# Kernel tuning notes

Hardware: AMD Instinct MI355X
Metric: run time of the kernel (lower is better)

## Reference

```python
import jax, jax.numpy as jnp
import numpy as np
import math

B, S, E = 2, 2048, 1024
H, D = 16, 64
LAMBDA_INIT = 0.8
GN_EPS = 1e-5


def setup_inputs() -> dict:
    key = jax.random.key(0)
    ks = jax.random.split(key, 12)
    s = 0.02
    inputs = jax.random.normal(ks[0], (B, S, E), jnp.float32)
    attention_mask = jnp.ones((B, S), jnp.float32)
    token_indices = jnp.sort(jax.random.randint(ks[1], (B, S), 0, S), axis=-1)
    Wq = jax.random.normal(ks[2], (2 * H * D, E), jnp.float32) * s
    Wk = jax.random.normal(ks[3], (2 * H * D, E), jnp.float32) * s
    Wv = jax.random.normal(ks[4], (H * D, E), jnp.float32) * s
    Wo = jax.random.normal(ks[5], (E, H * D), jnp.float32) * s
    lam_q1 = jax.random.normal(ks[6], (D,), jnp.float32) * 0.1
    lam_q2 = jax.random.normal(ks[7], (D,), jnp.float32) * 0.1
    lam_k1 = jax.random.normal(ks[8], (D,), jnp.float32) * 0.1
    lam_k2 = jax.random.normal(ks[9], (D,), jnp.float32) * 0.1
    gn_w = jnp.ones((H * D,), jnp.float32)
    gn_b = jnp.zeros((H * D,), jnp.float32)
    return dict(inputs=inputs, attention_mask=attention_mask, token_indices=token_indices,
                Wq=Wq, Wk=Wk, Wv=Wv, Wo=Wo,
                lam_q1=lam_q1, lam_q2=lam_q2, lam_k1=lam_k1, lam_k2=lam_k2,
                gn_w=gn_w, gn_b=gn_b)


def reference(inputs, attention_mask, token_indices, Wq, Wk, Wv, Wo,
              lam_q1, lam_q2, lam_k1, lam_k2, gn_w, gn_b):
    b, s, e = inputs.shape
    # projections: q,k have doubled head dim (differential), v is standard
    q = (inputs @ Wq.T).reshape(b, s, H, 2 * D).transpose(0, 2, 1, 3)  # [B,H,S,2D]
    k = (inputs @ Wk.T).reshape(b, s, H, 2 * D).transpose(0, 2, 1, 3)
    v = (inputs @ Wv.T).reshape(b, s, H, D).transpose(0, 2, 1, 3)      # [B,H,S,D]
    Q1, Q2 = q[..., :D], q[..., D:]
    K1, K2 = k[..., :D], k[..., D:]
    scale = 1.0 / math.sqrt(D)
    s1 = jnp.einsum('bhqd,bhkd->bhqk', Q1, K1) * scale
    s2 = jnp.einsum('bhqd,bhkd->bhqk', Q2, K2) * scale
    # ALiBi bias: slopes[h] * (pos_q - pos_k), subtracted
    slopes = 2.0 ** (-8.0 * jnp.arange(1, H + 1, dtype=jnp.float32) / H)
    pos = token_indices.astype(jnp.float32)                            # [B,S]
    pos_diff = pos[:, :, None] - pos[:, None, :]                       # [B,S,S]
    bias = slopes[None, :, None, None] * pos_diff[:, None, :, :]       # [B,H,S,S]
    # causal + padding masks
    causal = jnp.triu(jnp.full((s, s), -1e9, jnp.float32), 1)[None, None]
    pad = (1.0 - attention_mask)[:, None, None, :] * -1e9
    s1 = s1 - bias + causal + pad
    s2 = s2 - bias + causal + pad
    w1 = jax.nn.softmax(s1, axis=-1)
    w2 = jax.nn.softmax(s2, axis=-1)
    lam = jnp.exp(jnp.dot(lam_q1, lam_k1)) - jnp.exp(jnp.dot(lam_q2, lam_k2)) + LAMBDA_INIT
    w = w1 - lam * w2
    out = jnp.einsum('bhqk,bhkd->bhqd', w, v)                          # [B,H,S,D]
    # GroupNorm(num_groups=H, num_channels=H*D) over channels-first layout [B,C,S]
    x = out.transpose(0, 2, 1, 3).reshape(b, s, H * D).transpose(0, 2, 1)  # [B,C,S]
    xg = x.reshape(b, H, D * s)
    mean = xg.mean(axis=-1, keepdims=True)
    var = xg.var(axis=-1, keepdims=True)
    xn = ((xg - mean) / jnp.sqrt(var + GN_EPS)).reshape(b, H * D, s)
    xn = xn * gn_w[None, :, None] + gn_b[None, :, None]
    xn = xn * (1.0 - LAMBDA_INIT)
    attn = xn.transpose(0, 2, 1)                                       # [B,S,H*D]
    return attn @ Wo.T
```

## Files before the change

### kernel.cpp

```cpp
#include <hip/hip_runtime.h>
#include <hip/hip_bf16.h>

typedef __hip_bfloat16 bf16;
typedef float f32x4 __attribute__((ext_vector_type(4)));
typedef float fvec4 __attribute__((ext_vector_type(4)));
typedef short s16x8 __attribute__((ext_vector_type(8)));

#define NB_B 2
#define NB_S 2048
#define NB_E 1024
#define NB_H 16
#define NB_D 64

typedef const __attribute__((address_space(1))) void* GPTR;
typedef __attribute__((address_space(3))) void* LPTR;

__device__ __forceinline__ void gld16(const void* g, void* l) {
  __builtin_amdgcn_global_load_lds((GPTR)g, (LPTR)l, 16, 0, 0);
}

__device__ __forceinline__ s16x8 ld8(const bf16* p) { return *(const s16x8*)p; }

__device__ __forceinline__ f32x4 MFMA(s16x8 a, s16x8 b, f32x4 c) {
  return __builtin_amdgcn_mfma_f32_16x16x32_bf16(a, b, c, 0, 0, 0);
}

struct __align__(8) bf16x4 { bf16 a, b, c, d; };

__global__ void prep_kernel(const float* __restrict__ inputs,
                            const float* __restrict__ wq, const float* __restrict__ wk,
                            const float* __restrict__ wv, const float* __restrict__ wo,
                            const float* __restrict__ lq1, const float* __restrict__ lq2,
                            const float* __restrict__ lk1, const float* __restrict__ lk2,
                            bf16* __restrict__ xbf,
                            bf16* __restrict__ oq, bf16* __restrict__ ok,
                            bf16* __restrict__ ov, bf16* __restrict__ oo,
                            float* __restrict__ lamo) {
  const int blk = blockIdx.x;
  if (blk < 4096) {
    int i = blk * 256 + threadIdx.x;
    fvec4 v = ((const fvec4*)inputs)[i];
    bf16x4 o = { bf16(v.x), bf16(v.y), bf16(v.z), bf16(v.w) };
    ((bf16x4*)xbf)[i] = o;
  } else if (blk < 10240) {
    int i = (blk - 4096) * 256 + threadIdx.x;
    const float* src; bf16* dst; int off;
    if (i < 524288)       { src = wq; dst = oq; off = i; }
    else if (i < 1048576) { src = wk; dst = ok; off = i - 524288; }
    else if (i < 1310720) { src = wv; dst = ov; off = i - 1048576; }
    else                  { src = wo; dst = oo; off = i - 1310720; }
    fvec4 v = ((const fvec4*)src)[off];
    bf16x4 o = { bf16(v.x), bf16(v.y), bf16(v.z), bf16(v.w) };
    ((bf16x4*)dst)[off] = o;
  } else {
    int l = threadIdx.x;
    if (l < 64) {
      float d1 = lq1[l] * lk1[l];
      float d2 = lq2[l] * lk2[l];
#pragma unroll
      for (int o = 32; o; o >>= 1) { d1 += __shfl_xor(d1, o); d2 += __shfl_xor(d2, o); }
      if (l == 0) lamo[0] = expf(d1) - expf(d2) + 0.8f;
    }
  }
}

__global__ void combo_kernel(const int* __restrict__ tok, const float* __restrict__ amask,
                             float* __restrict__ combo) {
  int i = blockIdx.x * 256 + threadIdx.x;
  int hh = i >> 12, bs = i & 4095;
  float slopeL = exp2f(-0.5f * (float)(hh + 1)) * 1.44269504088896340736f;
  combo[i] = slopeL * (float)tok[bs] + (amask[bs] - 1.f) * 1.44269504e9f;
}

template <int EPI>
__global__ __launch_bounds__(256) void gemm_bt(const bf16* __restrict__ A,
                                               const bf16* __restrict__ Bw,
                                               bf16* __restrict__ Ob,
                                               bf16* __restrict__ Ob2,
                                               bf16* __restrict__ Ob3,
                                               float* __restrict__ Of,
                                               int Kd, float oscale) {
  __shared__ bf16 As[2][128 * 32];
  __shared__ bf16 Bs[2][128 * 32];
  const int tid = threadIdx.x;
  const int lane = tid & 63;
  const int fr = lane & 15, fq = lane >> 4;
  const int wave = tid >> 6;
  const int wr = (wave >> 1) * 64, wc = (wave & 1) * 64;
  const size_t m0 = (size_t)blockIdx.x * 128, n0 = (size_t)blockIdx.y * 128;

  f32x4 acc[4][4];
#pragma unroll
  for (int i = 0; i < 4; i++)
#pragma unroll
    for (int j = 0; j < 4; j++) acc[i][j] = f32x4{0.f, 0.f, 0.f, 0.f};

  const int ca = tid, cb = tid + 256;
  const bf16* ga0 = A + (m0 + (ca >> 2)) * Kd + (ca & 3) * 8;
  const bf16* ga1 = A + (m0 + (cb >> 2)) * Kd + (cb & 3) * 8;
  const bf16* gb0 = Bw + (n0 + (ca >> 2)) * Kd + (ca & 3) * 8;
  const bf16* gb1 = Bw + (n0 + (cb >> 2)) * Kd + (cb & 3) * 8;

  gld16(ga0, &As[0][ca * 8]);
  gld16(ga1, &As[0][cb * 8]);
  gld16(gb0, &Bs[0][ca * 8]);
  gld16(gb1, &Bs[0][cb * 8]);
  __syncthreads();

  const int NKT = Kd >> 5;
  for (int kti = 0; kti < NKT; ++kti) {
    const int cur = kti & 1;
    if (kti + 1 < NKT) {
      const int kt = (kti + 1) << 5;
      gld16(ga0 + kt, &As[cur ^ 1][ca * 8]);
      gld16(ga1 + kt, &As[cur ^ 1][cb * 8]);
      gld16(gb0 + kt, &Bs[cur ^ 1][ca * 8]);
      gld16(gb1 + kt, &Bs[cur ^ 1][cb * 8]);
    }
    s16x8 af[4], bfv[4];
#pragma unroll
    for (int mi = 0; mi < 4; mi++) af[mi] = ld8(&As[cur][(wr + mi * 16 + fr) * 32 + fq * 8]);
#pragma unroll
    for (int ni = 0; ni < 4; ni++) bfv[ni] = ld8(&Bs[cur][(wc + ni * 16 + fr) * 32 + fq * 8]);
#pragma unroll
    for (int mi = 0; mi < 4; mi++)
#pragma unroll
      for (int ni = 0; ni < 4; ni++)
        acc[mi][ni] = MFMA(af[mi], bfv[ni], acc[mi][ni]);
    __syncthreads();
  }

  bf16* dst = Ob;
  size_t nsub = 0;
  float osc = oscale;
  bool isV = false;
  if constexpr (EPI == 0) {
    if (n0 >= 4096)      { dst = Ob3; nsub = 4096; osc = 1.0f; isV = true; }
    else if (n0 >= 2048) { dst = Ob2; nsub = 2048; osc = 1.0f; }
  }

#pragma unroll
  for (int mi = 0; mi < 4; mi++)
#pragma unroll
    for (int ni = 0; ni < 4; ni++)
#pragma unroll
      for (int i = 0; i < 4; i++) {
        size_t m = m0 + wr + mi * 16 + fq * 4 + i;
        size_t n = n0 + wc + ni * 16 + fr;
        if constexpr (EPI == 0) {
          float v = acc[mi][ni][i] * osc;
          size_t nn = n - nsub;
          size_t b = m >> 11, s = m & 2047;
          if (!isV) {
            size_t h = nn >> 7, dd = nn & 127;
            dst[((b * NB_H + h) * NB_S + s) * 128 + dd] = bf16(v);
          } else {
            size_t h = nn >> 6, d = nn & 63;
            dst[((b * NB_H + h) * NB_D + d) * NB_S + s] = bf16(v);
          }
        } else {
          Of[m * 1024 + n] = acc[mi][ni][i] * oscale;
        }
      }
}

__global__ __launch_bounds__(512, 2) void attn_kernel(
    const bf16* __restrict__ Q, const bf16* __restrict__ Kk, const bf16* __restrict__ Vt,
    const int* __restrict__ tok, const float* __restrict__ combo,
    const float* __restrict__ lamp, bf16* __restrict__ Xb, float* __restrict__ gnp) {
  __shared__ bf16 Ks[2][2][4096];
  __shared__ bf16 Vs[2][4096];
  __shared__ bf16 Ps[8][1024];
  __shared__ float gs[8][2];

  const int tid = threadIdx.x, lane = tid & 63, wave = tid >> 6;
  const int fr = lane & 15, fq = lane >> 4;
  const int id = blockIdx.x;
  const int w = id >> 3;
  const int bh = (id & 7) * 4 + (w & 3);
  const int qj = 15 - (w >> 2);
  const int b = bh >> 4, h = bh & 15;

  const float lam = lamp[0];
  const float slopeL = exp2f(-0.5f * (float)(h + 1)) * 1.44269504088896340736f;
  const float* comboH = combo + ((size_t)h * NB_B + b) * NB_S;

  const bf16* Kbase = Kk + (size_t)bh * NB_S * 128;
  const bf16* Vbase = Vt + (size_t)bh * NB_D * NB_S;

  const s16x8 onesv = { 0x3F80, 0x3F80, 0x3F80, 0x3F80, 0x3F80, 0x3F80, 0x3F80, 0x3F80 };

  const bf16* gK[2]; int lK[2];
#pragma unroll
  for (int i = 0; i < 2; i++) {
    int c = tid + i * 512, set = c >> 9, cc = c & 511;
    int row = cc >> 3, col8 = cc & 7, sc = col8 ^ (row & 7);
    gK[i] = Kbase + (size_t)row * 128 + set * 64 + sc * 8;
    lK[i] = set * 4096 + cc * 8;
  }
  const bf16* gV; int lV;
  {
    int c = tid;
    int row = c >> 3, col8 = c & 7, sc = col8 ^ (row & 7);
    gV = Vbase + (size_t)row * NB_S + sc * 8;
    lV = c * 8;
  }

  const int q0 = qj * 128;
  const int qw = q0 + wave * 16;
  const int ntiles = 2 * qj + 2;

  const bf16* qrow = Q + ((size_t)bh * NB_S + qw + fr) * 128;
  s16x8 q1[2], q2[2];
  q1[0] = ld8(qrow + fq * 8);       q1[1] = ld8(qrow + 32 + fq * 8);
  q2[0] = ld8(qrow + 64 + fq * 8);  q2[1] = ld8(qrow + 96 + fq * 8);

  const int qg = qw + fr;
  const float pq = slopeL * (float)tok[b * NB_S + qg];

  float m1 = -1e30f, m2 = -1e30f;
  f32x4 acc1[4], acc2[4];
  f32x4 accL1 = f32x4{0.f,0.f,0.f,0.f}, accL2 = f32x4{0.f,0.f,0.f,0.f};
#pragma unroll
  for (int nt = 0; nt < 4; nt++) { acc1[nt] = f32x4{0.f,0.f,0.f,0.f}; acc2[nt] = f32x4{0.f,0.f,0.f,0.f}; }

#pragma unroll
  for (int i = 0; i < 2; i++) gld16(gK[i], &Ks[0][0][0] + lK[i]);
  gld16(gV, &Vs[0][0] + lV);
  __syncthreads();

  for (int t = 0; t < ntiles; ++t) {
    const int cur = t & 1;
    const int kv0 = t * 64;
    if (t + 1 < ntiles) {
#pragma unroll
      for (int i = 0; i < 2; i++)
        gld16(gK[i] + (size_t)(kv0 + 64) * 128, &Ks[cur ^ 1][0][0] + lK[i]);
      gld16(gV + (size_t)(kv0 + 64), &Vs[cur ^ 1][0] + lV);
    }

    const bool active = (kv0 <= qw + 15);
    if (active) {
      fvec4 cmbv[4];
#pragma unroll
      for (int nt = 0; nt < 4; nt++)
        cmbv[nt] = *(const fvec4*)(comboH + kv0 + nt * 16 + fq * 4);

      f32x4 c1[4], c2[4];
#pragma unroll
      for (int nt = 0; nt < 4; nt++) { c1[nt] = f32x4{0.f,0.f,0.f,0.f}; c2[nt] = f32x4{0.f,0.f,0.f,0.f}; }
      __builtin_amdgcn_s_setprio(1);
#pragma unroll
      for (int nt = 0; nt < 4; nt++) {
        const int krow = nt * 16 + fr;
#pragma unroll
        for (int kk = 0; kk < 2; kk++) {
          const int sch = ((kk * 4 + fq) ^ (krow & 7)) * 8;
          c1[nt] = MFMA(ld8(&Ks[cur][0][krow * 64 + sch]), q1[kk], c1[nt]);
          c2[nt] = MFMA(ld8(&Ks[cur][1][krow * 64 + sch]), q2[kk], c2[nt]);
        }
      }
      __builtin_amdgcn_s_setprio(0);

      float sv1[4][4], sv2[4][4];
#pragma unroll
      for (int nt = 0; nt < 4; nt++)
#pragma unroll
        for (int i = 0; i < 4; i++) {
          const float biasv = cmbv[nt][i] - pq;
          sv1[nt][i] = c1[nt][i] + biasv;
          sv2[nt][i] = c2[nt][i] + biasv;
        }
      if (kv0 + 63 > qw) {
#pragma unroll
        for (int nt = 0; nt < 4; nt++)
#pragma unroll
          for (int i = 0; i < 4; i++)
            if (kv0 + nt * 16 + fq * 4 + i > qg) { sv1[nt][i] = -1e30f; sv2[nt][i] = -1e30f; }
      }

      s16x8 vf[4][2];
#pragma unroll
      for (int nt = 0; nt < 4; nt++) {
        const int vrow = nt * 16 + fr;
#pragma unroll
        for (int kk = 0; kk < 2; kk++)
          vf[nt][kk] = ld8(&Vs[cur][vrow * 64 + (((kk * 4 + fq) ^ (vrow & 7)) << 3)]);
      }

      {
        float pm = fmaxf(fmaxf(fmaxf(sv1[0][0], sv1[0][1]), fmaxf(sv1[0][2], sv1[0][3])),
                         fmaxf(fmaxf(sv1[1][0], sv1[1][1]), fmaxf(sv1[1][2], sv1[1][3])));
        pm = fmaxf(pm, fmaxf(fmaxf(fmaxf(sv1[2][0], sv1[2][1]), fmaxf(sv1[2][2], sv1[2][3])),
                             fmaxf(fmaxf(sv1[3][0], sv1[3][1]), fmaxf(sv1[3][2], sv1[3][3]))));
        pm = fmaxf(pm, __shfl_xor(pm, 16));
        pm = fmaxf(pm, __shfl_xor(pm, 32));
        if (__any(pm > m1 + 8.f)) {
          const float nm = fmaxf(m1, pm);
          const float cor = exp2f(m1 - nm);
          m1 = nm;
#pragma unroll
          for (int i = 0; i < 4; i++) {
            const float ci = __shfl(cor, fq * 4 + i);
            accL1[i] *= ci;
#pragma unroll
            for (int nt = 0; nt < 4; nt++) acc1[nt][i] *= ci;
          }
        }
#pragma unroll
        for (int nt = 0; nt < 4; nt++) {
          bf16x4 pk = { bf16(exp2f(sv1[nt][0] - m1)), bf16(exp2f(sv1[nt][1] - m1)),
                        bf16(exp2f(sv1[nt][2] - m1)), bf16(exp2f(sv1[nt][3] - m1)) };
          *(bf16x4*)&Ps[wave][fr * 64 + ((((nt * 4 + fq) ^ ((fr & 7) << 1))) << 2)] = pk;
        }
        __builtin_amdgcn_s_setprio(1);
#pragma unroll
        for (int kk = 0; kk < 2; kk++) {
          const s16x8 pa = ld8(&Ps[wave][fr * 64 + (((kk * 8 + fq * 2) ^ ((fr & 7) << 1)) << 2)]);
          accL1 = MFMA(pa, onesv, accL1);
#pragma unroll
          for (int nt = 0; nt < 4; nt++) acc1[nt] = MFMA(pa, vf[nt][kk], acc1[nt]);
        }
        __builtin_amdgcn_s_setprio(0);
      }
      {
        float pm = fmaxf(fmaxf(fmaxf(sv2[0][0], sv2[0][1]), fmaxf(sv2[0][2], sv2[0][3])),
                         fmaxf(fmaxf(sv2[1][0], sv2[1][1]), fmaxf(sv2[1][2], sv2[1][3])));
        pm = fmaxf(pm, fmaxf(fmaxf(fmaxf(sv2[2][0], sv2[2][1]), fmaxf(sv2[2][2], sv2[2][3])),
                             fmaxf(fmaxf(sv2[3][0], sv2[3][1]), fmaxf(sv2[3][2], sv2[3][3]))));
        pm = fmaxf(pm, __shfl_xor(pm, 16));
        pm = fmaxf(pm, __shfl_xor(pm, 32));
        if (__any(pm > m2 + 8.f)) {
          const float nm = fmaxf(m2, pm);
          const float cor = exp2f(m2 - nm);
          m2 = nm;
#pragma unroll
          for (int i = 0; i < 4; i++) {
            const float ci = __shfl(cor, fq * 4 + i);
            accL2[i] *= ci;
#pragma unroll
            for (int nt = 0; nt < 4; nt++) acc2[nt][i] *= ci;
          }
        }
#pragma unroll
        for (int nt = 0; nt < 4; nt++) {
          bf16x4 pk = { bf16(exp2f(sv2[nt][0] - m2)), bf16(exp2f(sv2[nt][1] - m2)),
                        bf16(exp2f(sv2[nt][2] - m2)), bf16(exp2f(sv2[nt][3] - m2)) };
          *(bf16x4*)&Ps[wave][fr * 64 + ((((nt * 4 + fq) ^ ((fr & 7) << 1))) << 2)] = pk;
        }
        __builtin_amdgcn_s_setprio(1);
#pragma unroll
        for (int kk = 0; kk < 2; kk++) {
          const s16x8 pa = ld8(&Ps[wave][fr * 64 + (((kk * 8 + fq * 2) ^ ((fr & 7) << 1)) << 2)]);
          accL2 = MFMA(pa, onesv, accL2);
#pragma unroll
          for (int nt = 0; nt < 4; nt++) acc2[nt] = MFMA(pa, vf[nt][kk], acc2[nt]);
        }
        __builtin_amdgcn_s_setprio(0);
      }
    }

    __syncthreads();
  }

  float r1b[4], r2b[4];
#pragma unroll
  for (int i = 0; i < 4; i++) { r1b[i] = 1.f / accL1[i]; r2b[i] = lam / accL2[i]; }
  float s = 0.f, s2 = 0.f;
#pragma unroll
  for (int nt = 0; nt < 4; nt++)
#pragma unroll
    for (int i = 0; i < 4; i++) {
      const float v = acc1[nt][i] * r1b[i] - acc2[nt][i] * r2b[i];
      Xb[((size_t)bh * NB_S + qw + fq * 4 + i) * NB_D + nt * 16 + fr] = bf16(v);
      s += v; s2 += v * v;
    }
#pragma unroll
  for (int o = 32; o; o >>= 1) { s += __shfl_xor(s, o); s2 += __shfl_xor(s2, o); }
  if (lane == 0) { gs[wave][0] = s; gs[wave][1] = s2; }
  __syncthreads();
  if (tid == 0) {
    float S = 0.f, S2 = 0.f;
#pragma unroll
    for (int i = 0; i < 8; i++) { S += gs[i][0]; S2 += gs[i][1]; }
    atomicAdd(&gnp[bh * 2], S);
    atomicAdd(&gnp[bh * 2 + 1], S2);
  }
}

__global__ __launch_bounds__(256) void gn_apply(const bf16* __restrict__ Xb,
                                                const float* __restrict__ gnp,
                                                const float* __restrict__ gw,
                                                const float* __restrict__ gb,
                                                bf16* __restrict__ Xn) {
  const int blk = blockIdx.x, bh = blk >> 3, seg = blk & 7;
  const int b = bh >> 4, h = bh & 15;
  const float mean = gnp[bh * 2] * (1.f / 131072.f);
  const float var = gnp[bh * 2 + 1] * (1.f / 131072.f) - mean * mean;
  const float rstd = rsqrtf(var + 1e-5f) * 0.2f;
  const int tid = threadIdx.x;
  const int d0 = (tid * 8) & 63;
  const int c = h * 64 + d0;
  fvec4 w0 = *(const fvec4*)(gw + c), w1 = *(const fvec4*)(gw + c + 4);
  fvec4 b0 = *(const fvec4*)(gb + c), b1 = *(const fvec4*)(gb + c + 4);
  float wv[8] = { w0.x, w0.y, w0.z, w0.w, w1.x, w1.y, w1.z, w1.w };
  float bv[8] = { b0.x, b0.y, b0.z, b0.w, b1.x, b1.y, b1.z, b1.w };
  const bf16* xp = Xb + (size_t)bh * 131072;
#pragma unroll
  for (int j = 0; j < 8; j++) {
    const int e = seg * 16384 + (tid + j * 256) * 8;
    const int srow = e >> 6;
    s16x8 xv = *(const s16x8*)(xp + e);
    bf16 o8[8];
#pragma unroll
    for (int k = 0; k < 8; k++) {
      const float xf = __uint_as_float(((unsigned)(unsigned short)xv[k]) << 16);
      o8[k] = bf16((xf - mean) * rstd * wv[k] + 0.2f * bv[k]);
    }
    *(s16x8*)(Xn + ((size_t)b * NB_S + srow) * 1024 + c) = *(const s16x8*)o8;
  }
}

extern "C" void kernel_launch(void* const* d_in, const int* in_sizes, int n_in,
                              void* d_out, int out_size, void* d_ws, size_t ws_size,
                              hipStream_t stream) {
  const float* inputs = (const float*)d_in[0];
  const float* amask  = (const float*)d_in[1];
  const int*   tok    = (const int*)d_in[2];
  const float* Wq = (const float*)d_in[3];
  const float* Wk = (const float*)d_in[4];
  const float* Wv = (const float*)d_in[5];
  const float* Wo = (const float*)d_in[6];
  const float* lq1 = (const float*)d_in[7];
  const float* lq2 = (const float*)d_in[8];
  const float* lk1 = (const float*)d_in[9];
  const float* lk2 = (const float*)d_in[10];
  const float* gw = (const float*)d_in[11];
  const float* gb = (const float*)d_in[12];
  float* out = (float*)d_out;
  char* ws = (char*)d_ws;

  bf16* Xbf = (bf16*)(ws + 0);
  bf16* Wqb = (bf16*)(ws + 8388608);
  bf16* Wkb = (bf16*)(ws + 12582912);
  bf16* Wvb = (bf16*)(ws + 16777216);
  bf16* Xb  = (bf16*)(ws + 0);
  float* combo = (float*)(ws + 16777216);
  bf16* Qb  = (bf16*)(ws + 18874368);
  bf16* Xn  = (bf16*)(ws + 18874368);
  bf16* Kb  = (bf16*)(ws + 35651584);
  bf16* Vtb = (bf16*)(ws + 52428800);
  bf16* Wob = (bf16*)(ws + 60817408);
  float* lam = (float*)(ws + 62914560);
  float* gnp = (float*)(ws + 62914816);

  const float QSCALE = 0.125f * 1.44269504088896340736f;

  (void)hipMemsetAsync(gnp, 0, 512, stream);
  prep_kernel<<<10241, 256, 0, stream>>>(inputs, Wq, Wk, Wv, Wo, lq1, lq2, lk1, lk2,
                                         Xbf, Wqb, Wkb, Wvb, Wob, lam);

  gemm_bt<0><<<dim3(32, 40), 256, 0, stream>>>(Xbf, Wqb, Qb, Kb, Vtb, nullptr, 1024, QSCALE);

  combo_kernel<<<256, 256, 0, stream>>>(tok, amask, combo);

  attn_kernel<<<512, 512, 0, stream>>>(Qb, Kb, Vtb, tok, combo, lam, Xb, gnp);

  gn_apply<<<256, 256, 0, stream>>>(Xb, gnp, gw, gb, Xn);

  gemm_bt<2><<<dim3(32, 8), 256, 0, stream>>>(Xn, Wob, nullptr, nullptr, nullptr, out, 1024, 1.0f);
}
```

Measured before the change: 217.1 us.

## Fold ALiBi bias into MFMA accumulator init and remap GEMM blocks per XCD

In the attention kernel, the per-query ALiBi term is dropped, since a constant shift per row leaves the softmax unchanged. The score accumulators are seeded with the per-key combo bias, and the combo values for the next tile are prefetched into registers alongside the K/V loads. This removes the separate bias-add pass and the tok load. The GEMM kernels move to a 1D grid whose block index is remapped so each XCD works on a contiguous slice of N columns, aiming for better L2 reuse of weight tiles. Scores now carry larger absolute magnitudes without the query offset, which costs some float precision in the logits.

```diff
diff --git a/kernel.cpp b/kernel.cpp
--- a/kernel.cpp
+++ b/kernel.cpp
@@ -72,7 +72,7 @@
   combo[i] = slopeL * (float)tok[bs] + (amask[bs] - 1.f) * 1.44269504e9f;
 }
 
-template <int EPI>
+template <int EPI, int NYP>
 __global__ __launch_bounds__(256) void gemm_bt(const bf16* __restrict__ A,
                                                const bf16* __restrict__ Bw,
                                                bf16* __restrict__ Ob,
@@ -87,13 +87,16 @@
   const int fr = lane & 15, fq = lane >> 4;
   const int wave = tid >> 6;
   const int wr = (wave >> 1) * 64, wc = (wave & 1) * 64;
-  const size_t m0 = (size_t)blockIdx.x * 128, n0 = (size_t)blockIdx.y * 128;
+  const int idg = blockIdx.x;
+  const int xcd = idg & 7, j = idg >> 3;
+  const size_t m0 = (size_t)(j / NYP) * 128;
+  const size_t n0 = (size_t)(xcd * NYP + (j % NYP)) * 128;
 
   f32x4 acc[4][4];
 #pragma unroll
   for (int i = 0; i < 4; i++)
 #pragma unroll
-    for (int j = 0; j < 4; j++) acc[i][j] = f32x4{0.f, 0.f, 0.f, 0.f};
+    for (int jj = 0; jj < 4; jj++) acc[i][jj] = f32x4{0.f, 0.f, 0.f, 0.f};
 
   const int ca = tid, cb = tid + 256;
   const bf16* ga0 = A + (m0 + (ca >> 2)) * Kd + (ca & 3) * 8;
@@ -166,7 +169,7 @@
 
 __global__ __launch_bounds__(512, 2) void attn_kernel(
     const bf16* __restrict__ Q, const bf16* __restrict__ Kk, const bf16* __restrict__ Vt,
-    const int* __restrict__ tok, const float* __restrict__ combo,
+    const float* __restrict__ combo,
     const float* __restrict__ lamp, bf16* __restrict__ Xb, float* __restrict__ gnp) {
   __shared__ bf16 Ks[2][2][4096];
   __shared__ bf16 Vs[2][4096];
@@ -182,7 +185,6 @@
   const int b = bh >> 4, h = bh & 15;
 
   const float lam = lamp[0];
-  const float slopeL = exp2f(-0.5f * (float)(h + 1)) * 1.44269504088896340736f;
   const float* comboH = combo + ((size_t)h * NB_B + b) * NB_S;
 
   const bf16* Kbase = Kk + (size_t)bh * NB_S * 128;
@@ -216,7 +218,6 @@
   q2[0] = ld8(qrow + 64 + fq * 8);  q2[1] = ld8(qrow + 96 + fq * 8);
 
   const int qg = qw + fr;
-  const float pq = slopeL * (float)tok[b * NB_S + qg];
 
   float m1 = -1e30f, m2 = -1e30f;
   f32x4 acc1[4], acc2[4];
@@ -227,28 +228,30 @@
 #pragma unroll
   for (int i = 0; i < 2; i++) gld16(gK[i], &Ks[0][0][0] + lK[i]);
   gld16(gV, &Vs[0][0] + lV);
+  fvec4 cmb[4];
+#pragma unroll
+  for (int nt = 0; nt < 4; nt++) cmb[nt] = *(const fvec4*)(comboH + nt * 16 + fq * 4);
   __syncthreads();
 
   for (int t = 0; t < ntiles; ++t) {
     const int cur = t & 1;
     const int kv0 = t * 64;
+    fvec4 cnx[4];
     if (t + 1 < ntiles) {
 #pragma unroll
       for (int i = 0; i < 2; i++)
         gld16(gK[i] + (size_t)(kv0 + 64) * 128, &Ks[cur ^ 1][0][0] + lK[i]);
       gld16(gV + (size_t)(kv0 + 64), &Vs[cur ^ 1][0] + lV);
+#pragma unroll
+      for (int nt = 0; nt < 4; nt++)
+        cnx[nt] = *(const fvec4*)(comboH + kv0 + 64 + nt * 16 + fq * 4);
     }
 
     const bool active = (kv0 <= qw + 15);
     if (active) {
-      fvec4 cmbv[4];
-#pragma unroll
-      for (int nt = 0; nt < 4; nt++)
-        cmbv[nt] = *(const fvec4*)(comboH + kv0 + nt * 16 + fq * 4);
-
       f32x4 c1[4], c2[4];
 #pragma unroll
-      for (int nt = 0; nt < 4; nt++) { c1[nt] = f32x4{0.f,0.f,0.f,0.f}; c2[nt] = f32x4{0.f,0.f,0.f,0.f}; }
+      for (int nt = 0; nt < 4; nt++) { c1[nt] = cmb[nt]; c2[nt] = cmb[nt]; }
       __builtin_amdgcn_s_setprio(1);
 #pragma unroll
       for (int nt = 0; nt < 4; nt++) {
@@ -262,21 +265,12 @@
       }
       __builtin_amdgcn_s_setprio(0);
 
-      float sv1[4][4], sv2[4][4];
-#pragma unroll
-      for (int nt = 0; nt < 4; nt++)
-#pragma unroll
-        for (int i = 0; i < 4; i++) {
-          const float biasv = cmbv[nt][i] - pq;
-          sv1[nt][i] = c1[nt][i] + biasv;
-          sv2[nt][i] = c2[nt][i] + biasv;
-        }
       if (kv0 + 63 > qw) {
 #pragma unroll
         for (int nt = 0; nt < 4; nt++)
 #pragma unroll
           for (int i = 0; i < 4; i++)
-            if (kv0 + nt * 16 + fq * 4 + i > qg) { sv1[nt][i] = -1e30f; sv2[nt][i] = -1e30f; }
+            if (kv0 + nt * 16 + fq * 4 + i > qg) { c1[nt][i] = -1e30f; c2[nt][i] = -1e30f; }
       }
 
       s16x8 vf[4][2];
@@ -289,10 +283,10 @@
       }
 
       {
-        float pm = fmaxf(fmaxf(fmaxf(sv1[0][0], sv1[0][1]), fmaxf(sv1[0][2], sv1[0][3])),
-                         fmaxf(fmaxf(sv1[1][0], sv1[1][1]), fmaxf(sv1[1][2], sv1[1][3])));
-        pm = fmaxf(pm, fmaxf(fmaxf(fmaxf(sv1[2][0], sv1[2][1]), fmaxf(sv1[2][2], sv1[2][3])),
-                             fmaxf(fmaxf(sv1[3][0], sv1[3][1]), fmaxf(sv1[3][2], sv1[3][3]))));
+        float pm = fmaxf(fmaxf(fmaxf(c1[0][0], c1[0][1]), fmaxf(c1[0][2], c1[0][3])),
+                         fmaxf(fmaxf(c1[1][0], c1[1][1]), fmaxf(c1[1][2], c1[1][3])));
+        pm = fmaxf(pm, fmaxf(fmaxf(fmaxf(c1[2][0], c1[2][1]), fmaxf(c1[2][2], c1[2][3])),
+                             fmaxf(fmaxf(c1[3][0], c1[3][1]), fmaxf(c1[3][2], c1[3][3]))));
         pm = fmaxf(pm, __shfl_xor(pm, 16));
         pm = fmaxf(pm, __shfl_xor(pm, 32));
         if (__any(pm > m1 + 8.f)) {
@@ -309,8 +303,8 @@
         }
 #pragma unroll
         for (int nt = 0; nt < 4; nt++) {
-          bf16x4 pk = { bf16(exp2f(sv1[nt][0] - m1)), bf16(exp2f(sv1[nt][1] - m1)),
-                        bf16(exp2f(sv1[nt][2] - m1)), bf16(exp2f(sv1[nt][3] - m1)) };
+          bf16x4 pk = { bf16(exp2f(c1[nt][0] - m1)), bf16(exp2f(c1[nt][1] - m1)),
+                        bf16(exp2f(c1[nt][2] - m1)), bf16(exp2f(c1[nt][3] - m1)) };
           *(bf16x4*)&Ps[wave][fr * 64 + ((((nt * 4 + fq) ^ ((fr & 7) << 1))) << 2)] = pk;
         }
         __builtin_amdgcn_s_setprio(1);
@@ -324,10 +318,10 @@
         __builtin_amdgcn_s_setprio(0);
       }
       {
-        float pm = fmaxf(fmaxf(fmaxf(sv2[0][0], sv2[0][1]), fmaxf(sv2[0][2], sv2[0][3])),
-                         fmaxf(fmaxf(sv2[1][0], sv2[1][1]), fmaxf(sv2[1][2], sv2[1][3])));
-        pm = fmaxf(pm, fmaxf(fmaxf(fmaxf(sv2[2][0], sv2[2][1]), fmaxf(sv2[2][2], sv2[2][3])),
-                             fmaxf(fmaxf(sv2[3][0], sv2[3][1]), fmaxf(sv2[3][2], sv2[3][3]))));
+        float pm = fmaxf(fmaxf(fmaxf(c2[0][0], c2[0][1]), fmaxf(c2[0][2], c2[0][3])),
+                         fmaxf(fmaxf(c2[1][0], c2[1][1]), fmaxf(c2[1][2], c2[1][3])));
+        pm = fmaxf(pm, fmaxf(fmaxf(fmaxf(c2[2][0], c2[2][1]), fmaxf(c2[2][2], c2[2][3])),
+                             fmaxf(fmaxf(c2[3][0], c2[3][1]), fmaxf(c2[3][2], c2[3][3]))));
         pm = fmaxf(pm, __shfl_xor(pm, 16));
         pm = fmaxf(pm, __shfl_xor(pm, 32));
         if (__any(pm > m2 + 8.f)) {
@@ -344,8 +338,8 @@
         }
 #pragma unroll
         for (int nt = 0; nt < 4; nt++) {
-          bf16x4 pk = { bf16(exp2f(sv2[nt][0] - m2)), bf16(exp2f(sv2[nt][1] - m2)),
-                        bf16(exp2f(sv2[nt][2] - m2)), bf16(exp2f(sv2[nt][3] - m2)) };
+          bf16x4 pk = { bf16(exp2f(c2[nt][0] - m2)), bf16(exp2f(c2[nt][1] - m2)),
+                        bf16(exp2f(c2[nt][2] - m2)), bf16(exp2f(c2[nt][3] - m2)) };
           *(bf16x4*)&Ps[wave][fr * 64 + ((((nt * 4 + fq) ^ ((fr & 7) << 1))) << 2)] = pk;
         }
         __builtin_amdgcn_s_setprio(1);
@@ -360,6 +354,8 @@
       }
     }
 
+#pragma unroll
+    for (int nt = 0; nt < 4; nt++) cmb[nt] = cnx[nt];
     __syncthreads();
   }
 
@@ -407,8 +403,8 @@
   float bv[8] = { b0.x, b0.y, b0.z, b0.w, b1.x, b1.y, b1.z, b1.w };
   const bf16* xp = Xb + (size_t)bh * 131072;
 #pragma unroll
-  for (int j = 0; j < 8; j++) {
-    const int e = seg * 16384 + (tid + j * 256) * 8;
+  for (int jj = 0; jj < 8; jj++) {
+    const int e = seg * 16384 + (tid + jj * 256) * 8;
     const int srow = e >> 6;
     s16x8 xv = *(const s16x8*)(xp + e);
     bf16 o8[8];
@@ -460,13 +456,13 @@
   prep_kernel<<<10241, 256, 0, stream>>>(inputs, Wq, Wk, Wv, Wo, lq1, lq2, lk1, lk2,
                                          Xbf, Wqb, Wkb, Wvb, Wob, lam);
 
-  gemm_bt<0><<<dim3(32, 40), 256, 0, stream>>>(Xbf, Wqb, Qb, Kb, Vtb, nullptr, 1024, QSCALE);
+  gemm_bt<0, 5><<<1280, 256, 0, stream>>>(Xbf, Wqb, Qb, Kb, Vtb, nullptr, 1024, QSCALE);
 
   combo_kernel<<<256, 256, 0, stream>>>(tok, amask, combo);
 
-  attn_kernel<<<512, 512, 0, stream>>>(Qb, Kb, Vtb, tok, combo, lam, Xb, gnp);
+  attn_kernel<<<512, 512, 0, stream>>>(Qb, Kb, Vtb, combo, lam, Xb, gnp);
 
   gn_apply<<<256, 256, 0, stream>>>(Xb, gnp, gw, gb, Xn);
 
-  gemm_bt<2><<<dim3(32, 8), 256, 0, stream>>>(Xn, Wob, nullptr, nullptr, nullptr, out, 1024, 1.0f);
-}
+  gemm_bt<2, 1><<<256, 256, 0, stream>>>(Xn, Wob, nullptr, nullptr, nullptr, out, 1024, 1.0f);
+}
```

Result: slower. 233.2 us (+7.4%).
